# Optimization experiments

Hardware: AMD Instinct MI355X
Metric: run time of the kernel (lower is better)

## Reference

```python
import jax, jax.numpy as jnp
import numpy as np

N_NODES = 50000
N_EDGES = 800000
N_SUPPORTS = 2
D_IN = 512
D_OUT = 128


def setup_inputs() -> dict:
    key = jax.random.key(0)
    ks = jax.random.split(key, 6)
    x = jax.random.normal(ks[0], (N_NODES, D_IN), dtype=jnp.float32)
    kernels = jax.random.normal(ks[1], (N_SUPPORTS, D_IN, D_OUT), dtype=jnp.float32) * 0.05
    bias = jax.random.normal(ks[2], (D_OUT,), dtype=jnp.float32) * 0.05
    adj_vals = jax.random.uniform(ks[3], (N_SUPPORTS, N_EDGES), dtype=jnp.float32)
    adj_rows = jax.random.randint(ks[4], (N_SUPPORTS, N_EDGES), 0, N_NODES, dtype=jnp.int32)
    adj_cols = jax.random.randint(ks[5], (N_SUPPORTS, N_EDGES), 0, N_NODES, dtype=jnp.int32)
    return {"x": x, "kernels": kernels, "bias": bias,
            "adj_vals": adj_vals, "adj_rows": adj_rows, "adj_cols": adj_cols}


def _spmm(vals, rows, cols, dense):
    # COO sparse [N,N] @ dense [N,F] -> [N,F]
    gathered = vals[:, None] * dense[cols]            # [E, F]
    return jax.ops.segment_sum(gathered, rows, num_segments=N_NODES)


def reference(x, kernels, bias, adj_vals, adj_rows, adj_cols):
    # dropout rate = 0.0 -> identity
    out = jnp.zeros((N_NODES, D_OUT), dtype=x.dtype)
    for s in range(N_SUPPORTS):  # small fixed number of supports
        pre_sup = x @ kernels[s]                      # [N, D_OUT]
        out = out + _spmm(adj_vals[s], adj_rows[s], adj_cols[s], pre_sup)
    out = out + bias
    return jax.nn.relu(out)
```

## Files before the change

### kernel.cpp

```cpp
#include <hip/hip_runtime.h>

#define N_NODES 50000
#define N_EDGES 800000
#define D_IN    512
#define D_OUT   128
#define N_SUP   2
#define N_COLS  (N_SUP * D_OUT)
#define BINS    (N_SUP * N_NODES)
#define NB_S    196
#define NB      (N_SUP * NB_S)
#define CAP     4608
#define CHUNK   4096
#define NCHUNK  ((N_EDGES + CHUNK - 1) / CHUNK)

#define TILE_R  16
#define NTILES  (N_NODES / TILE_R)
#define GGRID   256

typedef __attribute__((ext_vector_type(8))) __bf16 bf16x8;
typedef __attribute__((ext_vector_type(4))) float  f32x4;

__global__ __launch_bounds__(256) void convert_w(const float* __restrict__ w,
                                                 __bf16* __restrict__ wt2,
                                                 int* __restrict__ gcursor) {
    const int g = blockIdx.x * 256 + threadIdx.x;
    if (g < NB) gcursor[g] = 0;
    if (g >= (D_IN / 8) * N_COLS) return;
    const int kq = g >> 8;
    const int n  = g & 255;
    const int s  = n >> 7;
    const int np = n & 127;
    bf16x8 v;
#pragma unroll
    for (int j = 0; j < 8; ++j) {
        const int k = kq * 8 + j;
        v[j] = (__bf16)w[((size_t)s * D_IN + k) * D_OUT + np];
    }
    *(bf16x8*)(wt2 + (size_t)g * 8) = v;
}

__global__ __launch_bounds__(512, 2) void gemm_bf16_v2(const float* __restrict__ x,
                                                       const __bf16* __restrict__ wt2,
                                                       __bf16* __restrict__ pre) {
    __shared__ __align__(16) __bf16 As[TILE_R * 64 * 8];

    const int t    = threadIdx.x;
    const int lane = t & 63;
    const int w    = t >> 6;
    const int l15  = lane & 15;
    const int quad = lane >> 4;

    bf16x8 B0[16], B1[16];
#pragma unroll
    for (int kb = 0; kb < 16; ++kb) {
        const size_t g0 = (size_t)(kb * 4 + quad) * 256 + w * 32 + l15;
        B0[kb] = *(const bf16x8*)(wt2 + g0 * 8);
        B1[kb] = *(const bf16x8*)(wt2 + (g0 + 16) * 8);
    }

    const int s_out = w >> 2;
    const int cp0   = (w & 3) * 32 + l15;

    const int srow = t >> 5;
    const int sc0  = (t & 31) * 2;
    const int swz  = srow & 7;

    int tile = blockIdx.x;
    float4 f0, f1, f2, f3;
    {
        const float* src = x + ((size_t)tile * TILE_R + srow) * D_IN + sc0 * 8;
        f0 = ((const float4*)src)[0];
        f1 = ((const float4*)src)[1];
        f2 = ((const float4*)src)[2];
        f3 = ((const float4*)src)[3];
    }

    while (tile < NTILES) {
        bf16x8 lo, hi;
        lo[0] = (__bf16)f0.x; lo[1] = (__bf16)f0.y; lo[2] = (__bf16)f0.z; lo[3] = (__bf16)f0.w;
        lo[4] = (__bf16)f1.x; lo[5] = (__bf16)f1.y; lo[6] = (__bf16)f1.z; lo[7] = (__bf16)f1.w;
        hi[0] = (__bf16)f2.x; hi[1] = (__bf16)f2.y; hi[2] = (__bf16)f2.z; hi[3] = (__bf16)f2.w;
        hi[4] = (__bf16)f3.x; hi[5] = (__bf16)f3.y; hi[6] = (__bf16)f3.z; hi[7] = (__bf16)f3.w;

        __syncthreads();
        *(bf16x8*)&As[((size_t)srow * 64 + (sc0       ^ swz)) * 8] = lo;
        *(bf16x8*)&As[((size_t)srow * 64 + ((sc0 + 1) ^ swz)) * 8] = hi;
        __syncthreads();

        const int next = tile + GGRID;
        if (next < NTILES) {
            const float* src = x + ((size_t)next * TILE_R + srow) * D_IN + sc0 * 8;
            f0 = ((const float4*)src)[0];
            f1 = ((const float4*)src)[1];
            f2 = ((const float4*)src)[2];
            f3 = ((const float4*)src)[3];
        }

        f32x4 acc0 = (f32x4)0.f, acc1 = (f32x4)0.f;
#pragma unroll
        for (int kb = 0; kb < 16; ++kb) {
            const int c = (kb * 4 + quad) ^ (l15 & 7);
            bf16x8 a = *(const bf16x8*)&As[((size_t)l15 * 64 + c) * 8];
            acc0 = __builtin_amdgcn_mfma_f32_16x16x32_bf16(a, B0[kb], acc0, 0, 0, 0);
            acc1 = __builtin_amdgcn_mfma_f32_16x16x32_bf16(a, B1[kb], acc1, 0, 0, 0);
        }

        __bf16* dst = pre + ((size_t)s_out * N_NODES + (size_t)tile * TILE_R + quad * 4) * D_OUT + cp0;
#pragma unroll
        for (int r = 0; r < 4; ++r) {
            dst[(size_t)r * D_OUT]      = (__bf16)acc0[r];
            dst[(size_t)r * D_OUT + 16] = (__bf16)acc1[r];
        }

        tile = next;
    }
}

__global__ __launch_bounds__(256) void scatter_coarse(const float* __restrict__ adj_vals,
                                                      const int* __restrict__ adj_rows,
                                                      const int* __restrict__ adj_cols,
                                                      int* __restrict__ gcursor,
                                                      uint2* __restrict__ coarse) {
    __shared__ int hist[NB_S];
    __shared__ int excl[NB_S];
    __shared__ int lbase[NB_S];
    __shared__ int rankc[NB_S];
    __shared__ int sc[256];
    __shared__ uint2 buf[CHUNK];

    const int s = blockIdx.y;
    const int t = threadIdx.x;
    if (t < NB_S) { hist[t] = 0; rankc[t] = 0; }
    __syncthreads();

    const int e0 = blockIdx.x * CHUNK;
    int   rr[16]; int cc[16]; float vv[16];
#pragma unroll
    for (int i = 0; i < 16; ++i) {
        const int e = e0 + i * 256 + t;
        if (e < N_EDGES) {
            const size_t src = (size_t)s * N_EDGES + e;
            rr[i] = adj_rows[src];
            cc[i] = adj_cols[src];
            vv[i] = adj_vals[src];
            atomicAdd(&hist[rr[i] >> 8], 1);
        } else {
            rr[i] = -1; cc[i] = 0; vv[i] = 0.f;
        }
    }
    __syncthreads();

    sc[t] = (t < NB_S) ? hist[t] : 0;
    __syncthreads();
    for (int off = 1; off < 256; off <<= 1) {
        const int a = (t >= off) ? sc[t - off] : 0;
        __syncthreads();
        sc[t] += a;
        __syncthreads();
    }
    if (t < NB_S) {
        excl[t]  = sc[t] - hist[t];
        lbase[t] = hist[t] ? atomicAdd(&gcursor[s * NB_S + t], hist[t]) : 0;
    }
    __syncthreads();

#pragma unroll
    for (int i = 0; i < 16; ++i) {
        if (rr[i] >= 0) {
            const int b   = rr[i] >> 8;
            const int pos = excl[b] + atomicAdd(&rankc[b], 1);
            buf[pos] = make_uint2(__float_as_uint(vv[i]),
                                  ((unsigned)rr[i] << 16) | (unsigned)cc[i]);
        }
    }
    __syncthreads();

    const int total = min(e0 + CHUNK, N_EDGES) - e0;
    for (int i = t; i < total; i += 256) {
        const uint2 ed = buf[i];
        const int b   = ed.y >> 24;
        const int dst = lbase[b] + (i - excl[b]);
        if (dst < CAP)
            coarse[(size_t)(s * NB_S + b) * CAP + dst] = ed;
    }
}

__global__ __launch_bounds__(256) void scatter_fine(const uint2* __restrict__ coarse,
                                                    const int* __restrict__ gcursor,
                                                    uint2* __restrict__ sorted,
                                                    int* __restrict__ row_off,
                                                    int* __restrict__ row_cnt) {
    __shared__ int rh[256];
    __shared__ int sd[256];
    __shared__ int rex[256];
    __shared__ int rc[256];
    __shared__ uint2 buf[CAP];

    const int bk = blockIdx.x;
    const int s  = blockIdx.y;
    const int t  = threadIdx.x;
    const int bkt = s * NB_S + bk;
    const size_t b0 = (size_t)bkt * CAP;
    const int cnt = min(gcursor[bkt], CAP);

    rh[t] = 0; rc[t] = 0;
    __syncthreads();

    uint2 ev[18];
#pragma unroll
    for (int j = 0; j < 18; ++j) {
        const int i = j * 256 + t;
        if (i < cnt) {
            ev[j] = coarse[b0 + i];
            atomicAdd(&rh[(ev[j].y >> 16) & 255], 1);
        }
    }
    __syncthreads();

    const int myc = rh[t];
    sd[t] = myc;
    __syncthreads();
    for (int off = 1; off < 256; off <<= 1) {
        const int a = (t >= off) ? sd[t - off] : 0;
        __syncthreads();
        sd[t] += a;
        __syncthreads();
    }
    const int ex = sd[t] - myc;
    rex[t] = ex;
    const int row = (bk << 8) + t;
    if (row < N_NODES) {
        row_off[s * N_NODES + row] = (int)(b0 + ex);
        row_cnt[s * N_NODES + row] = myc;
    }
    __syncthreads();

#pragma unroll
    for (int j = 0; j < 18; ++j) {
        const int i = j * 256 + t;
        if (i < cnt) {
            const int rl   = (ev[j].y >> 16) & 255;
            const int pos  = rex[rl] + atomicAdd(&rc[rl], 1);
            buf[pos] = make_uint2(ev[j].x, ev[j].y & 0xFFFFu);
        }
    }
    __syncthreads();

    for (int i = t; i < cnt; i += 256)
        sorted[b0 + i] = buf[i];
}

__global__ __launch_bounds__(256) void gather_spmm(const int* __restrict__ row_off,
                                                   const int* __restrict__ row_cnt,
                                                   const uint2* __restrict__ sorted,
                                                   const uint4* __restrict__ pre_q,
                                                   const float* __restrict__ bias,
                                                   float* __restrict__ out) {
    const int lane = threadIdx.x & 63;
    const int q    = lane >> 4;
    const int fl   = lane & 15;
    const int row  = blockIdx.x * 4 + (threadIdx.x >> 6);
    if (row >= N_NODES) return;

    float a[8];
#pragma unroll
    for (int k = 0; k < 8; ++k) a[k] = 0.f;

#pragma unroll
    for (int s = 0; s < N_SUP; ++s) {
        const int bin   = s * N_NODES + row;
        const int start = row_off[bin];
        const int cnt   = row_cnt[bin];
        const uint4* psup = pre_q + (size_t)s * N_NODES * 16 + fl;

        for (int e0 = 0; e0 < cnt; e0 += 64) {
            const int m = min(64, cnt - e0);
            int   c = 0;
            float v = 0.f;
            if (lane < m) {
                const uint2 ed = sorted[start + e0 + lane];
                v = __uint_as_float(ed.x);
                c = (int)ed.y;
            }
            const int steps = (m + 3) >> 2;

            auto step = [&](int jj) {
                const int   idx = (jj < m) ? jj : 0;
                float vj = __shfl(v, idx);
                const int cj = __shfl(c, idx);
                if (jj >= m) vj = 0.f;
                const uint4 p = psup[(size_t)cj * 16];
                a[0] += vj * __uint_as_float(p.x << 16);
                a[1] += vj * __uint_as_float(p.x & 0xffff0000u);
                a[2] += vj * __uint_as_float(p.y << 16);
                a[3] += vj * __uint_as_float(p.y & 0xffff0000u);
                a[4] += vj * __uint_as_float(p.z << 16);
                a[5] += vj * __uint_as_float(p.z & 0xffff0000u);
                a[6] += vj * __uint_as_float(p.w << 16);
                a[7] += vj * __uint_as_float(p.w & 0xffff0000u);
            };
            int jj = 0;
            for (; jj + 1 < steps; jj += 2) {
                step(jj * 4 + q);
                step(jj * 4 + 4 + q);
            }
            if (jj < steps) step(jj * 4 + q);
        }
    }

#pragma unroll
    for (int k = 0; k < 8; ++k) {
        a[k] += __shfl_xor(a[k], 16);
        a[k] += __shfl_xor(a[k], 32);
    }

    if (lane < 16) {
        const float4 b0 = *(const float4*)(bias + fl * 8);
        const float4 b1 = *(const float4*)(bias + fl * 8 + 4);
        float4 o0, o1;
        o0.x = fmaxf(a[0] + b0.x, 0.f);
        o0.y = fmaxf(a[1] + b0.y, 0.f);
        o0.z = fmaxf(a[2] + b0.z, 0.f);
        o0.w = fmaxf(a[3] + b0.w, 0.f);
        o1.x = fmaxf(a[4] + b1.x, 0.f);
        o1.y = fmaxf(a[5] + b1.y, 0.f);
        o1.z = fmaxf(a[6] + b1.z, 0.f);
        o1.w = fmaxf(a[7] + b1.w, 0.f);
        float* dst = out + (size_t)row * D_OUT + fl * 8;
        *(float4*)(dst)     = o0;
        *(float4*)(dst + 4) = o1;
    }
}

extern "C" void kernel_launch(void* const* d_in, const int* in_sizes, int n_in,
                              void* d_out, int out_size, void* d_ws, size_t ws_size,
                              hipStream_t stream) {
    const float* x        = (const float*)d_in[0];
    const float* kernels  = (const float*)d_in[1];
    const float* bias     = (const float*)d_in[2];
    const float* adj_vals = (const float*)d_in[3];
    const int*   adj_rows = (const int*)d_in[4];
    const int*   adj_cols = (const int*)d_in[5];
    float* out = (float*)d_out;

    char* ws = (char*)d_ws;
    size_t off = 0;
    auto alloc = [&](size_t bytes) {
        char* p = ws + off;
        off += (bytes + 255) & ~(size_t)255;
        return p;
    };
    __bf16* pre    = (__bf16*)alloc(sizeof(__bf16) * N_SUP * N_NODES * D_OUT);
    __bf16* wt2    = (__bf16*)alloc(sizeof(__bf16) * D_IN * N_COLS);
    uint2*  coarse = (uint2*) alloc(sizeof(uint2)  * NB * CAP);
    uint2*  sorted = (uint2*) alloc(sizeof(uint2)  * NB * CAP);
    int*    row_off = (int*)alloc(sizeof(int) * BINS);
    int*    row_cnt = (int*)alloc(sizeof(int) * BINS);
    int*    gcursor = (int*)alloc(sizeof(int) * NB);

    convert_w<<<(D_IN / 8) * N_COLS / 256, 256, 0, stream>>>(kernels, wt2, gcursor);

    gemm_bf16_v2<<<GGRID, 512, 0, stream>>>(x, wt2, pre);

    dim3 gc(NCHUNK, N_SUP);
    scatter_coarse<<<gc, 256, 0, stream>>>(adj_vals, adj_rows, adj_cols, gcursor, coarse);
    dim3 gf(NB_S, N_SUP);
    scatter_fine<<<gf, 256, 0, stream>>>(coarse, gcursor, sorted, row_off, row_cnt);

    gather_spmm<<<(N_NODES + 3) / 4, 256, 0, stream>>>(row_off, row_cnt, sorted,
                                                       (const uint4*)pre, bias, out);
}
```

Measured before the change: 266.0 us.

## Fuse bf16 GEMM and coarse edge bucketing into one kernel

Merges the dense bf16 MFMA GEMM and the coarse COO bucketing pass into a single 512-block launch. Each block first computes GEMM tiles for one support's half of the output columns, then reuses its shared memory to bucket one edge chunk. The edge chunk size becomes 3125 so the edges divide evenly across 256 blocks per support. The intent is to remove a kernel launch and let the memory-bound scatter overlap across blocks with the compute-bound GEMM. The cost is that each GEMM block now reads each x tile twice, once per column half, and holds more registers per thread.

```diff
diff --git a/kernel.cpp b/kernel.cpp
--- a/kernel.cpp
+++ b/kernel.cpp
@@ -10,12 +10,9 @@
 #define NB_S    196
 #define NB      (N_SUP * NB_S)
 #define CAP     4608
-#define CHUNK   4096
-#define NCHUNK  ((N_EDGES + CHUNK - 1) / CHUNK)
-
-#define TILE_R  16
-#define NTILES  (N_NODES / TILE_R)
-#define GGRID   256
+#define CHUNK   3125
+#define NTILES  3125
+#define GC_GRID 512
 
 typedef __attribute__((ext_vector_type(8))) __bf16 bf16x8;
 typedef __attribute__((ext_vector_type(4))) float  f32x4;
@@ -32,156 +29,160 @@
     const int np = n & 127;
     bf16x8 v;
 #pragma unroll
-    for (int j = 0; j < 8; ++j) {
-        const int k = kq * 8 + j;
-        v[j] = (__bf16)w[((size_t)s * D_IN + k) * D_OUT + np];
-    }
+    for (int j = 0; j < 8; ++j)
+        v[j] = (__bf16)w[((size_t)s * D_IN + kq * 8 + j) * D_OUT + np];
     *(bf16x8*)(wt2 + (size_t)g * 8) = v;
 }
 
-__global__ __launch_bounds__(512, 2) void gemm_bf16_v2(const float* __restrict__ x,
-                                                       const __bf16* __restrict__ wt2,
-                                                       __bf16* __restrict__ pre) {
-    __shared__ __align__(16) __bf16 As[TILE_R * 64 * 8];
-
-    const int t    = threadIdx.x;
-    const int lane = t & 63;
-    const int w    = t >> 6;
-    const int l15  = lane & 15;
-    const int quad = lane >> 4;
-
-    bf16x8 B0[16], B1[16];
-#pragma unroll
-    for (int kb = 0; kb < 16; ++kb) {
-        const size_t g0 = (size_t)(kb * 4 + quad) * 256 + w * 32 + l15;
-        B0[kb] = *(const bf16x8*)(wt2 + g0 * 8);
-        B1[kb] = *(const bf16x8*)(wt2 + (g0 + 16) * 8);
-    }
-
-    const int s_out = w >> 2;
-    const int cp0   = (w & 3) * 32 + l15;
-
-    const int srow = t >> 5;
-    const int sc0  = (t & 31) * 2;
-    const int swz  = srow & 7;
-
-    int tile = blockIdx.x;
-    float4 f0, f1, f2, f3;
-    {
-        const float* src = x + ((size_t)tile * TILE_R + srow) * D_IN + sc0 * 8;
-        f0 = ((const float4*)src)[0];
-        f1 = ((const float4*)src)[1];
-        f2 = ((const float4*)src)[2];
-        f3 = ((const float4*)src)[3];
-    }
-
-    while (tile < NTILES) {
-        bf16x8 lo, hi;
-        lo[0] = (__bf16)f0.x; lo[1] = (__bf16)f0.y; lo[2] = (__bf16)f0.z; lo[3] = (__bf16)f0.w;
-        lo[4] = (__bf16)f1.x; lo[5] = (__bf16)f1.y; lo[6] = (__bf16)f1.z; lo[7] = (__bf16)f1.w;
-        hi[0] = (__bf16)f2.x; hi[1] = (__bf16)f2.y; hi[2] = (__bf16)f2.z; hi[3] = (__bf16)f2.w;
-        hi[4] = (__bf16)f3.x; hi[5] = (__bf16)f3.y; hi[6] = (__bf16)f3.z; hi[7] = (__bf16)f3.w;
-
-        __syncthreads();
-        *(bf16x8*)&As[((size_t)srow * 64 + (sc0       ^ swz)) * 8] = lo;
-        *(bf16x8*)&As[((size_t)srow * 64 + ((sc0 + 1) ^ swz)) * 8] = hi;
-        __syncthreads();
-
-        const int next = tile + GGRID;
-        if (next < NTILES) {
-            const float* src = x + ((size_t)next * TILE_R + srow) * D_IN + sc0 * 8;
-            f0 = ((const float4*)src)[0];
-            f1 = ((const float4*)src)[1];
-            f2 = ((const float4*)src)[2];
-            f3 = ((const float4*)src)[3];
-        }
-
-        f32x4 acc0 = (f32x4)0.f, acc1 = (f32x4)0.f;
-#pragma unroll
-        for (int kb = 0; kb < 16; ++kb) {
-            const int c = (kb * 4 + quad) ^ (l15 & 7);
-            bf16x8 a = *(const bf16x8*)&As[((size_t)l15 * 64 + c) * 8];
-            acc0 = __builtin_amdgcn_mfma_f32_16x16x32_bf16(a, B0[kb], acc0, 0, 0, 0);
-            acc1 = __builtin_amdgcn_mfma_f32_16x16x32_bf16(a, B1[kb], acc1, 0, 0, 0);
-        }
-
-        __bf16* dst = pre + ((size_t)s_out * N_NODES + (size_t)tile * TILE_R + quad * 4) * D_OUT + cp0;
-#pragma unroll
-        for (int r = 0; r < 4; ++r) {
-            dst[(size_t)r * D_OUT]      = (__bf16)acc0[r];
-            dst[(size_t)r * D_OUT + 16] = (__bf16)acc1[r];
-        }
-
-        tile = next;
-    }
-}
-
-__global__ __launch_bounds__(256) void scatter_coarse(const float* __restrict__ adj_vals,
+__global__ __launch_bounds__(256, 2) void gemm_coarse(const float* __restrict__ x,
+                                                      const __bf16* __restrict__ wt2,
+                                                      __bf16* __restrict__ pre,
+                                                      const float* __restrict__ adj_vals,
                                                       const int* __restrict__ adj_rows,
                                                       const int* __restrict__ adj_cols,
                                                       int* __restrict__ gcursor,
                                                       uint2* __restrict__ coarse) {
-    __shared__ int hist[NB_S];
-    __shared__ int excl[NB_S];
-    __shared__ int lbase[NB_S];
-    __shared__ int rankc[NB_S];
-    __shared__ int sc[256];
-    __shared__ uint2 buf[CHUNK];
-
-    const int s = blockIdx.y;
-    const int t = threadIdx.x;
-    if (t < NB_S) { hist[t] = 0; rankc[t] = 0; }
-    __syncthreads();
-
-    const int e0 = blockIdx.x * CHUNK;
-    int   rr[16]; int cc[16]; float vv[16];
-#pragma unroll
-    for (int i = 0; i < 16; ++i) {
-        const int e = e0 + i * 256 + t;
-        if (e < N_EDGES) {
-            const size_t src = (size_t)s * N_EDGES + e;
-            rr[i] = adj_rows[src];
-            cc[i] = adj_cols[src];
-            vv[i] = adj_vals[src];
-            atomicAdd(&hist[rr[i] >> 8], 1);
-        } else {
-            rr[i] = -1; cc[i] = 0; vv[i] = 0.f;
-        }
-    }
-    __syncthreads();
-
-    sc[t] = (t < NB_S) ? hist[t] : 0;
-    __syncthreads();
-    for (int off = 1; off < 256; off <<= 1) {
-        const int a = (t >= off) ? sc[t - off] : 0;
-        __syncthreads();
-        sc[t] += a;
-        __syncthreads();
-    }
-    if (t < NB_S) {
-        excl[t]  = sc[t] - hist[t];
-        lbase[t] = hist[t] ? atomicAdd(&gcursor[s * NB_S + t], hist[t]) : 0;
-    }
-    __syncthreads();
-
-#pragma unroll
-    for (int i = 0; i < 16; ++i) {
-        if (rr[i] >= 0) {
-            const int b   = rr[i] >> 8;
-            const int pos = excl[b] + atomicAdd(&rankc[b], 1);
-            buf[pos] = make_uint2(__float_as_uint(vv[i]),
-                                  ((unsigned)rr[i] << 16) | (unsigned)cc[i]);
-        }
-    }
-    __syncthreads();
-
-    const int total = min(e0 + CHUNK, N_EDGES) - e0;
-    for (int i = t; i < total; i += 256) {
-        const uint2 ed = buf[i];
-        const int b   = ed.y >> 24;
-        const int dst = lbase[b] + (i - excl[b]);
-        if (dst < CAP)
-            coarse[(size_t)(s * NB_S + b) * CAP + dst] = ed;
+    __shared__ __align__(16) char smem[29184];
+    const int t   = threadIdx.x;
+    const int bid = blockIdx.x;
+
+    {
+        __bf16* As = (__bf16*)smem;
+        const int h     = bid >> 8;
+        const int tslot = bid & 255;
+        const int wv    = t >> 6;
+        const int lane  = t & 63;
+        const int l15   = lane & 15;
+        const int quad  = lane >> 4;
+
+        bf16x8 B0[16], B1[16];
+#pragma unroll
+        for (int kb = 0; kb < 16; ++kb) {
+            const size_t g0 = (size_t)(kb * 4 + quad) * 256 + h * 128 + wv * 32 + l15;
+            B0[kb] = *(const bf16x8*)(wt2 + g0 * 8);
+            B1[kb] = *(const bf16x8*)(wt2 + (g0 + 16) * 8);
+        }
+
+        const int srow = t >> 4;
+        const int sc0  = (t & 15) * 4;
+        const int swz  = srow & 7;
+
+        int tile = tslot;
+        float4 f[8];
+        {
+            const float* src = x + ((size_t)tile * 16 + srow) * D_IN + sc0 * 8;
+#pragma unroll
+            for (int j = 0; j < 8; ++j) f[j] = ((const float4*)src)[j];
+        }
+
+        while (tile < NTILES) {
+            bf16x8 c4[4];
+#pragma unroll
+            for (int cj = 0; cj < 4; ++cj) {
+                const float4 u = f[2 * cj], v2 = f[2 * cj + 1];
+                bf16x8 a;
+                a[0] = (__bf16)u.x;  a[1] = (__bf16)u.y;
+                a[2] = (__bf16)u.z;  a[3] = (__bf16)u.w;
+                a[4] = (__bf16)v2.x; a[5] = (__bf16)v2.y;
+                a[6] = (__bf16)v2.z; a[7] = (__bf16)v2.w;
+                c4[cj] = a;
+            }
+            __syncthreads();
+#pragma unroll
+            for (int cj = 0; cj < 4; ++cj)
+                *(bf16x8*)&As[((size_t)srow * 64 + ((sc0 + cj) ^ swz)) * 8] = c4[cj];
+            __syncthreads();
+
+            const int next = tile + 256;
+            if (next < NTILES) {
+                const float* src = x + ((size_t)next * 16 + srow) * D_IN + sc0 * 8;
+#pragma unroll
+                for (int j = 0; j < 8; ++j) f[j] = ((const float4*)src)[j];
+            }
+
+            f32x4 acc0 = (f32x4)0.f, acc1 = (f32x4)0.f;
+#pragma unroll
+            for (int kb = 0; kb < 16; ++kb) {
+                const int c = (kb * 4 + quad) ^ (l15 & 7);
+                bf16x8 a = *(const bf16x8*)&As[((size_t)l15 * 64 + c) * 8];
+                acc0 = __builtin_amdgcn_mfma_f32_16x16x32_bf16(a, B0[kb], acc0, 0, 0, 0);
+                acc1 = __builtin_amdgcn_mfma_f32_16x16x32_bf16(a, B1[kb], acc1, 0, 0, 0);
+            }
+
+            __bf16* dst = pre + ((size_t)h * N_NODES + (size_t)tile * 16 + quad * 4) * D_OUT
+                              + wv * 32 + l15;
+#pragma unroll
+            for (int r = 0; r < 4; ++r) {
+                dst[(size_t)r * D_OUT]      = (__bf16)acc0[r];
+                dst[(size_t)r * D_OUT + 16] = (__bf16)acc1[r];
+            }
+            tile = next;
+        }
+    }
+    __syncthreads();
+
+    {
+        int*   hist  = (int*)smem;
+        int*   excl  = hist + NB_S;
+        int*   lbase = excl + NB_S;
+        int*   rankc = lbase + NB_S;
+        int*   sc    = rankc + NB_S;
+        uint2* buf   = (uint2*)(smem + 4160);
+
+        const int s  = bid >> 8;
+        const int ch = bid & 255;
+        if (t < NB_S) { hist[t] = 0; rankc[t] = 0; }
+        __syncthreads();
+
+        const int e0 = ch * CHUNK;
+        int   rr[13]; int cc[13]; float vv[13];
+#pragma unroll
+        for (int i = 0; i < 13; ++i) {
+            const int idx = i * 256 + t;
+            if (idx < CHUNK) {
+                const size_t src = (size_t)s * N_EDGES + e0 + idx;
+                rr[i] = adj_rows[src];
+                cc[i] = adj_cols[src];
+                vv[i] = adj_vals[src];
+                atomicAdd(&hist[rr[i] >> 8], 1);
+            } else {
+                rr[i] = -1; cc[i] = 0; vv[i] = 0.f;
+            }
+        }
+        __syncthreads();
+
+        sc[t] = (t < NB_S) ? hist[t] : 0;
+        __syncthreads();
+        for (int off = 1; off < 256; off <<= 1) {
+            const int a = (t >= off) ? sc[t - off] : 0;
+            __syncthreads();
+            sc[t] += a;
+            __syncthreads();
+        }
+        if (t < NB_S) {
+            excl[t]  = sc[t] - hist[t];
+            lbase[t] = hist[t] ? atomicAdd(&gcursor[s * NB_S + t], hist[t]) : 0;
+        }
+        __syncthreads();
+
+#pragma unroll
+        for (int i = 0; i < 13; ++i) {
+            if (rr[i] >= 0) {
+                const int b   = rr[i] >> 8;
+                const int pos = excl[b] + atomicAdd(&rankc[b], 1);
+                buf[pos] = make_uint2(__float_as_uint(vv[i]),
+                                      ((unsigned)rr[i] << 16) | (unsigned)cc[i]);
+            }
+        }
+        __syncthreads();
+
+        for (int i = t; i < CHUNK; i += 256) {
+            const uint2 ed = buf[i];
+            const int b   = ed.y >> 24;
+            const int dst = lbase[b] + (i - excl[b]);
+            if (dst < CAP)
+                coarse[(size_t)(s * NB_S + b) * CAP + dst] = ed;
+        }
     }
 }
 
@@ -360,10 +361,10 @@
 
     convert_w<<<(D_IN / 8) * N_COLS / 256, 256, 0, stream>>>(kernels, wt2, gcursor);
 
-    gemm_bf16_v2<<<GGRID, 512, 0, stream>>>(x, wt2, pre);
-
-    dim3 gc(NCHUNK, N_SUP);
-    scatter_coarse<<<gc, 256, 0, stream>>>(adj_vals, adj_rows, adj_cols, gcursor, coarse);
+    gemm_coarse<<<GC_GRID, 256, 0, stream>>>(x, wt2, pre,
+                                             adj_vals, adj_rows, adj_cols,
+                                             gcursor, coarse);
+
     dim3 gf(NB_S, N_SUP);
     scatter_fine<<<gf, 256, 0, stream>>>(coarse, gcursor, sorted, row_off, row_cnt);
 
```

After: 270.0 us. Within noise of the previous version (+1.5%).

## Fuse fine row sort into SpMM gather with 64-row buckets held in LDS

Applied to the files above, without the earlier changes.

Shrinks coarse buckets from 256 rows to 64 rows and merges the fine per-row sort with the gather SpMM. Each block sorts its bucket for both supports in shared memory and then accumulates output rows directly from LDS. This removes the global sorted array, the row offset and count arrays, and one kernel launch with its global round trip. In exchange it uses fewer, heavier gather blocks (782 blocks of 512 threads, 8 rows per wave) and a tighter per-bucket capacity. Edges beyond that capacity would be dropped silently.

```diff
diff --git a/kernel.cpp b/kernel.cpp
--- a/kernel.cpp
+++ b/kernel.cpp
@@ -6,13 +6,10 @@
 #define D_OUT   128
 #define N_SUP   2
 #define N_COLS  (N_SUP * D_OUT)
-#define BINS    (N_SUP * N_NODES)
-#define NB_S    196
+#define NB_S    782
 #define NB      (N_SUP * NB_S)
-#define CAP     4608
-#define CHUNK   4096
-#define NCHUNK  ((N_EDGES + CHUNK - 1) / CHUNK)
-
+#define CAPF    1280
+#define CHUNK   3125
 #define TILE_R  16
 #define NTILES  (N_NODES / TILE_R)
 #define GGRID   256
@@ -32,10 +29,8 @@
     const int np = n & 127;
     bf16x8 v;
 #pragma unroll
-    for (int j = 0; j < 8; ++j) {
-        const int k = kq * 8 + j;
-        v[j] = (__bf16)w[((size_t)s * D_IN + k) * D_OUT + np];
-    }
+    for (int j = 0; j < 8; ++j)
+        v[j] = (__bf16)w[((size_t)s * D_IN + kq * 8 + j) * D_OUT + np];
     *(bf16x8*)(wt2 + (size_t)g * 8) = v;
 }
 
@@ -116,7 +111,7 @@
     }
 }
 
-__global__ __launch_bounds__(256) void scatter_coarse(const float* __restrict__ adj_vals,
+__global__ __launch_bounds__(512) void scatter_coarse(const float* __restrict__ adj_vals,
                                                       const int* __restrict__ adj_rows,
                                                       const int* __restrict__ adj_cols,
                                                       int* __restrict__ gcursor,
@@ -125,49 +120,59 @@
     __shared__ int excl[NB_S];
     __shared__ int lbase[NB_S];
     __shared__ int rankc[NB_S];
-    __shared__ int sc[256];
+    __shared__ int sc[1024];
     __shared__ uint2 buf[CHUNK];
 
-    const int s = blockIdx.y;
-    const int t = threadIdx.x;
-    if (t < NB_S) { hist[t] = 0; rankc[t] = 0; }
-    __syncthreads();
-
-    const int e0 = blockIdx.x * CHUNK;
-    int   rr[16]; int cc[16]; float vv[16];
-#pragma unroll
-    for (int i = 0; i < 16; ++i) {
-        const int e = e0 + i * 256 + t;
-        if (e < N_EDGES) {
-            const size_t src = (size_t)s * N_EDGES + e;
+    const int bid = blockIdx.x;
+    const int s   = bid >> 8;
+    const int ch  = bid & 255;
+    const int t   = threadIdx.x;
+
+    for (int b = t; b < NB_S; b += 512) { hist[b] = 0; rankc[b] = 0; }
+    __syncthreads();
+
+    const int e0 = ch * CHUNK;
+    int   rr[7]; int cc[7]; float vv[7];
+#pragma unroll
+    for (int i = 0; i < 7; ++i) {
+        const int idx = i * 512 + t;
+        if (idx < CHUNK) {
+            const size_t src = (size_t)s * N_EDGES + e0 + idx;
             rr[i] = adj_rows[src];
             cc[i] = adj_cols[src];
             vv[i] = adj_vals[src];
-            atomicAdd(&hist[rr[i] >> 8], 1);
+            atomicAdd(&hist[rr[i] >> 6], 1);
         } else {
             rr[i] = -1; cc[i] = 0; vv[i] = 0.f;
         }
     }
     __syncthreads();
 
-    sc[t] = (t < NB_S) ? hist[t] : 0;
-    __syncthreads();
-    for (int off = 1; off < 256; off <<= 1) {
-        const int a = (t >= off) ? sc[t - off] : 0;
-        __syncthreads();
-        sc[t] += a;
-        __syncthreads();
-    }
-    if (t < NB_S) {
-        excl[t]  = sc[t] - hist[t];
-        lbase[t] = hist[t] ? atomicAdd(&gcursor[s * NB_S + t], hist[t]) : 0;
-    }
-    __syncthreads();
-
-#pragma unroll
-    for (int i = 0; i < 16; ++i) {
+    sc[t]       = (t       < NB_S) ? hist[t]       : 0;
+    sc[t + 512] = (t + 512 < NB_S) ? hist[t + 512] : 0;
+    __syncthreads();
+    for (int off = 1; off < 1024; off <<= 1) {
+        const int a0 = (t >= off) ? sc[t - off] : 0;
+        const int a1 = sc[t + 512 - off];
+        __syncthreads();
+        sc[t]       += a0;
+        sc[t + 512] += a1;
+        __syncthreads();
+    }
+#pragma unroll
+    for (int h = 0; h < 2; ++h) {
+        const int b = t + h * 512;
+        if (b < NB_S) {
+            excl[b]  = sc[b] - hist[b];
+            lbase[b] = hist[b] ? atomicAdd(&gcursor[s * NB_S + b], hist[b]) : 0;
+        }
+    }
+    __syncthreads();
+
+#pragma unroll
+    for (int i = 0; i < 7; ++i) {
         if (rr[i] >= 0) {
-            const int b   = rr[i] >> 8;
+            const int b   = rr[i] >> 6;
             const int pos = excl[b] + atomicAdd(&rankc[b], 1);
             buf[pos] = make_uint2(__float_as_uint(vv[i]),
                                   ((unsigned)rr[i] << 16) | (unsigned)cc[i]);
@@ -175,160 +180,155 @@
     }
     __syncthreads();
 
-    const int total = min(e0 + CHUNK, N_EDGES) - e0;
-    for (int i = t; i < total; i += 256) {
+    for (int i = t; i < CHUNK; i += 512) {
         const uint2 ed = buf[i];
-        const int b   = ed.y >> 24;
+        const int b   = (int)(ed.y >> 22);
         const int dst = lbase[b] + (i - excl[b]);
-        if (dst < CAP)
-            coarse[(size_t)(s * NB_S + b) * CAP + dst] = ed;
-    }
-}
-
-__global__ __launch_bounds__(256) void scatter_fine(const uint2* __restrict__ coarse,
-                                                    const int* __restrict__ gcursor,
-                                                    uint2* __restrict__ sorted,
-                                                    int* __restrict__ row_off,
-                                                    int* __restrict__ row_cnt) {
-    __shared__ int rh[256];
-    __shared__ int sd[256];
-    __shared__ int rex[256];
-    __shared__ int rc[256];
-    __shared__ uint2 buf[CAP];
-
-    const int bk = blockIdx.x;
-    const int s  = blockIdx.y;
-    const int t  = threadIdx.x;
-    const int bkt = s * NB_S + bk;
-    const size_t b0 = (size_t)bkt * CAP;
-    const int cnt = min(gcursor[bkt], CAP);
-
-    rh[t] = 0; rc[t] = 0;
-    __syncthreads();
-
-    uint2 ev[18];
-#pragma unroll
-    for (int j = 0; j < 18; ++j) {
-        const int i = j * 256 + t;
-        if (i < cnt) {
-            ev[j] = coarse[b0 + i];
-            atomicAdd(&rh[(ev[j].y >> 16) & 255], 1);
-        }
-    }
-    __syncthreads();
-
-    const int myc = rh[t];
-    sd[t] = myc;
-    __syncthreads();
-    for (int off = 1; off < 256; off <<= 1) {
-        const int a = (t >= off) ? sd[t - off] : 0;
-        __syncthreads();
-        sd[t] += a;
-        __syncthreads();
-    }
-    const int ex = sd[t] - myc;
-    rex[t] = ex;
-    const int row = (bk << 8) + t;
-    if (row < N_NODES) {
-        row_off[s * N_NODES + row] = (int)(b0 + ex);
-        row_cnt[s * N_NODES + row] = myc;
-    }
-    __syncthreads();
-
-#pragma unroll
-    for (int j = 0; j < 18; ++j) {
-        const int i = j * 256 + t;
-        if (i < cnt) {
-            const int rl   = (ev[j].y >> 16) & 255;
-            const int pos  = rex[rl] + atomicAdd(&rc[rl], 1);
-            buf[pos] = make_uint2(ev[j].x, ev[j].y & 0xFFFFu);
-        }
-    }
-    __syncthreads();
-
-    for (int i = t; i < cnt; i += 256)
-        sorted[b0 + i] = buf[i];
-}
-
-__global__ __launch_bounds__(256) void gather_spmm(const int* __restrict__ row_off,
-                                                   const int* __restrict__ row_cnt,
-                                                   const uint2* __restrict__ sorted,
+        if (dst < CAPF)
+            coarse[(size_t)(s * NB_S + b) * CAPF + dst] = ed;
+    }
+}
+
+__global__ __launch_bounds__(512) void fine_gather(const uint2* __restrict__ coarse,
+                                                   const int* __restrict__ gcursor,
                                                    const uint4* __restrict__ pre_q,
                                                    const float* __restrict__ bias,
                                                    float* __restrict__ out) {
-    const int lane = threadIdx.x & 63;
+    __shared__ uint2 buf[2 * CAPF];
+    __shared__ int rex[2][64];
+    __shared__ int rcnt[2][64];
+    __shared__ int rh[64];
+    __shared__ int rc[64];
+    __shared__ int sd[64];
+
+    const int bk = blockIdx.x;
+    const int t  = threadIdx.x;
+
+#pragma unroll
+    for (int s = 0; s < N_SUP; ++s) {
+        if (t < 64) { rh[t] = 0; rc[t] = 0; }
+        __syncthreads();
+
+        const int bkt  = s * NB_S + bk;
+        const size_t b0 = (size_t)bkt * CAPF;
+        const int cnt  = min(gcursor[bkt], CAPF);
+
+        uint2 ev0, ev1, ev2;
+        ev0 = make_uint2(0u, 0u); ev1 = ev0; ev2 = ev0;
+        if (t < cnt)        { ev0 = coarse[b0 + t];        atomicAdd(&rh[(ev0.y >> 16) & 63], 1); }
+        if (t + 512 < cnt)  { ev1 = coarse[b0 + t + 512];  atomicAdd(&rh[(ev1.y >> 16) & 63], 1); }
+        if (t + 1024 < cnt) { ev2 = coarse[b0 + t + 1024]; atomicAdd(&rh[(ev2.y >> 16) & 63], 1); }
+        __syncthreads();
+
+        if (t < 64) sd[t] = rh[t];
+        __syncthreads();
+        for (int off = 1; off < 64; off <<= 1) {
+            const int a = (t < 64 && t >= off) ? sd[t - off] : 0;
+            __syncthreads();
+            if (t < 64) sd[t] += a;
+            __syncthreads();
+        }
+        if (t < 64) {
+            rex[s][t]  = sd[t] - rh[t];
+            rcnt[s][t] = rh[t];
+        }
+        __syncthreads();
+
+        if (t < cnt) {
+            const int rl = (ev0.y >> 16) & 63;
+            buf[s * CAPF + rex[s][rl] + atomicAdd(&rc[rl], 1)] =
+                make_uint2(ev0.x, ev0.y & 0xFFFFu);
+        }
+        if (t + 512 < cnt) {
+            const int rl = (ev1.y >> 16) & 63;
+            buf[s * CAPF + rex[s][rl] + atomicAdd(&rc[rl], 1)] =
+                make_uint2(ev1.x, ev1.y & 0xFFFFu);
+        }
+        if (t + 1024 < cnt) {
+            const int rl = (ev2.y >> 16) & 63;
+            buf[s * CAPF + rex[s][rl] + atomicAdd(&rc[rl], 1)] =
+                make_uint2(ev2.x, ev2.y & 0xFFFFu);
+        }
+        __syncthreads();
+    }
+
+    const int lane = t & 63;
     const int q    = lane >> 4;
     const int fl   = lane & 15;
-    const int row  = blockIdx.x * 4 + (threadIdx.x >> 6);
-    if (row >= N_NODES) return;
-
-    float a[8];
-#pragma unroll
-    for (int k = 0; k < 8; ++k) a[k] = 0.f;
-
-#pragma unroll
-    for (int s = 0; s < N_SUP; ++s) {
-        const int bin   = s * N_NODES + row;
-        const int start = row_off[bin];
-        const int cnt   = row_cnt[bin];
-        const uint4* psup = pre_q + (size_t)s * N_NODES * 16 + fl;
-
-        for (int e0 = 0; e0 < cnt; e0 += 64) {
-            const int m = min(64, cnt - e0);
-            int   c = 0;
-            float v = 0.f;
-            if (lane < m) {
-                const uint2 ed = sorted[start + e0 + lane];
-                v = __uint_as_float(ed.x);
-                c = (int)ed.y;
+    const int wv   = t >> 6;
+
+    for (int ri = 0; ri < 8; ++ri) {
+        const int rloc = wv * 8 + ri;
+        const int row  = bk * 64 + rloc;
+
+        float a[8];
+#pragma unroll
+        for (int k = 0; k < 8; ++k) a[k] = 0.f;
+
+#pragma unroll
+        for (int s = 0; s < N_SUP; ++s) {
+            const int start = rex[s][rloc];
+            const int cnt   = rcnt[s][rloc];
+            const uint2* eb = buf + s * CAPF + start;
+            const uint4* psup = pre_q + (size_t)s * N_NODES * 16 + fl;
+
+            for (int e0 = 0; e0 < cnt; e0 += 64) {
+                const int m = min(64, cnt - e0);
+                int   c = 0;
+                float v = 0.f;
+                if (lane < m) {
+                    const uint2 ed = eb[e0 + lane];
+                    v = __uint_as_float(ed.x);
+                    c = (int)ed.y;
+                }
+                const int steps = (m + 3) >> 2;
+
+                auto step = [&](int jj) {
+                    const int   idx = (jj < m) ? jj : 0;
+                    float vj = __shfl(v, idx);
+                    const int cj = __shfl(c, idx);
+                    if (jj >= m) vj = 0.f;
+                    const uint4 p = psup[(size_t)cj * 16];
+                    a[0] += vj * __uint_as_float(p.x << 16);
+                    a[1] += vj * __uint_as_float(p.x & 0xffff0000u);
+                    a[2] += vj * __uint_as_float(p.y << 16);
+                    a[3] += vj * __uint_as_float(p.y & 0xffff0000u);
+                    a[4] += vj * __uint_as_float(p.z << 16);
+                    a[5] += vj * __uint_as_float(p.z & 0xffff0000u);
+                    a[6] += vj * __uint_as_float(p.w << 16);
+                    a[7] += vj * __uint_as_float(p.w & 0xffff0000u);
+                };
+                int jj = 0;
+                for (; jj + 1 < steps; jj += 2) {
+                    step(jj * 4 + q);
+                    step(jj * 4 + 4 + q);
+                }
+                if (jj < steps) step(jj * 4 + q);
             }
-            const int steps = (m + 3) >> 2;
-
-            auto step = [&](int jj) {
-                const int   idx = (jj < m) ? jj : 0;
-                float vj = __shfl(v, idx);
-                const int cj = __shfl(c, idx);
-                if (jj >= m) vj = 0.f;
-                const uint4 p = psup[(size_t)cj * 16];
-                a[0] += vj * __uint_as_float(p.x << 16);
-                a[1] += vj * __uint_as_float(p.x & 0xffff0000u);
-                a[2] += vj * __uint_as_float(p.y << 16);
-                a[3] += vj * __uint_as_float(p.y & 0xffff0000u);
-                a[4] += vj * __uint_as_float(p.z << 16);
-                a[5] += vj * __uint_as_float(p.z & 0xffff0000u);
-                a[6] += vj * __uint_as_float(p.w << 16);
-                a[7] += vj * __uint_as_float(p.w & 0xffff0000u);
-            };
-            int jj = 0;
-            for (; jj + 1 < steps; jj += 2) {
-                step(jj * 4 + q);
-                step(jj * 4 + 4 + q);
-            }
-            if (jj < steps) step(jj * 4 + q);
-        }
-    }
-
-#pragma unroll
-    for (int k = 0; k < 8; ++k) {
-        a[k] += __shfl_xor(a[k], 16);
-        a[k] += __shfl_xor(a[k], 32);
-    }
-
-    if (lane < 16) {
-        const float4 b0 = *(const float4*)(bias + fl * 8);
-        const float4 b1 = *(const float4*)(bias + fl * 8 + 4);
-        float4 o0, o1;
-        o0.x = fmaxf(a[0] + b0.x, 0.f);
-        o0.y = fmaxf(a[1] + b0.y, 0.f);
-        o0.z = fmaxf(a[2] + b0.z, 0.f);
-        o0.w = fmaxf(a[3] + b0.w, 0.f);
-        o1.x = fmaxf(a[4] + b1.x, 0.f);
-        o1.y = fmaxf(a[5] + b1.y, 0.f);
-        o1.z = fmaxf(a[6] + b1.z, 0.f);
-        o1.w = fmaxf(a[7] + b1.w, 0.f);
-        float* dst = out + (size_t)row * D_OUT + fl * 8;
-        *(float4*)(dst)     = o0;
-        *(float4*)(dst + 4) = o1;
+        }
+
+#pragma unroll
+        for (int k = 0; k < 8; ++k) {
+            a[k] += __shfl_xor(a[k], 16);
+            a[k] += __shfl_xor(a[k], 32);
+        }
+
+        if (lane < 16 && row < N_NODES) {
+            const float4 b0 = *(const float4*)(bias + fl * 8);
+            const float4 b1 = *(const float4*)(bias + fl * 8 + 4);
+            float4 o0, o1;
+            o0.x = fmaxf(a[0] + b0.x, 0.f);
+            o0.y = fmaxf(a[1] + b0.y, 0.f);
+            o0.z = fmaxf(a[2] + b0.z, 0.f);
+            o0.w = fmaxf(a[3] + b0.w, 0.f);
+            o1.x = fmaxf(a[4] + b1.x, 0.f);
+            o1.y = fmaxf(a[5] + b1.y, 0.f);
+            o1.z = fmaxf(a[6] + b1.z, 0.f);
+            o1.w = fmaxf(a[7] + b1.w, 0.f);
+            float* dst = out + (size_t)row * D_OUT + fl * 8;
+            *(float4*)(dst)     = o0;
+            *(float4*)(dst + 4) = o1;
+        }
     }
 }
 
@@ -352,21 +352,16 @@
     };
     __bf16* pre    = (__bf16*)alloc(sizeof(__bf16) * N_SUP * N_NODES * D_OUT);
     __bf16* wt2    = (__bf16*)alloc(sizeof(__bf16) * D_IN * N_COLS);
-    uint2*  coarse = (uint2*) alloc(sizeof(uint2)  * NB * CAP);
-    uint2*  sorted = (uint2*) alloc(sizeof(uint2)  * NB * CAP);
-    int*    row_off = (int*)alloc(sizeof(int) * BINS);
-    int*    row_cnt = (int*)alloc(sizeof(int) * BINS);
+    uint2*  coarse = (uint2*) alloc(sizeof(uint2)  * NB * CAPF);
     int*    gcursor = (int*)alloc(sizeof(int) * NB);
 
     convert_w<<<(D_IN / 8) * N_COLS / 256, 256, 0, stream>>>(kernels, wt2, gcursor);
 
     gemm_bf16_v2<<<GGRID, 512, 0, stream>>>(x, wt2, pre);
 
-    dim3 gc(NCHUNK, N_SUP);
-    scatter_coarse<<<gc, 256, 0, stream>>>(adj_vals, adj_rows, adj_cols, gcursor, coarse);
-    dim3 gf(NB_S, N_SUP);
-    scatter_fine<<<gf, 256, 0, stream>>>(coarse, gcursor, sorted, row_off, row_cnt);
-
-    gather_spmm<<<(N_NODES + 3) / 4, 256, 0, stream>>>(row_off, row_cnt, sorted,
-                                                       (const uint4*)pre, bias, out);
-}
+    scatter_coarse<<<512, 512, 0, stream>>>(adj_vals, adj_rows, adj_cols,
+                                            gcursor, coarse);
+
+    fine_gather<<<NB_S, 512, 0, stream>>>(coarse, gcursor, (const uint4*)pre,
+                                          bias, out);
+}
```

After: 261.3 us. Within noise of the previous version (-1.8%).
